# Kernel optimization log

Hardware: AMD Instinct MI355X
Metric: run time of the kernel (lower is better)

## Reference

```python
import jax, jax.numpy as jnp
import numpy as np

STRIDE = 8
PAD = 8
KSZ = 16


def setup_inputs() -> dict:
    key = jax.random.key(0)
    k1, k2, k3 = jax.random.split(key, 3)
    B, Cin, Cout, L = 16, 512, 1, 4000
    inp = jax.random.normal(k1, (B, Cin, L), dtype=jnp.float32)
    # t60 in [0.1, 0.5) so that round(t60*100)-10 lands in [0, 40]
    t60s = 0.1 + 0.39 * jax.random.uniform(k2, (B // 2,), dtype=jnp.float32)
    kernel_weight = jax.random.uniform(k3, (41, Cin, Cout, KSZ), dtype=jnp.float32)
    return {"input": inp, "t60s": t60s, "kernel_weight": kernel_weight}


def reference(input, t60s, kernel_weight):
    # per-sample kernel index: round(t60*100).int().repeat(2) - 10
    idx = jnp.tile(jnp.round(t60s * 100.0).astype(jnp.int32), 2) - 10  # (B,)
    w = kernel_weight[idx]                      # (B, Cin, Cout, K) gathered per sample
    # torch conv_transpose1d(x, W) == conv(x with lhs_dilation=stride,
    #                                      flip_k(W).swap(Cin,Cout), pad=K-1-p)
    w = jnp.flip(jnp.swapaxes(w, 1, 2), axis=-1)  # (B, Cout, Cin, K)
    pad = KSZ - 1 - PAD

    def per_sample(x, wk):  # x: (Cin, L), wk: (Cout, Cin, K)
        y = jax.lax.conv_general_dilated(
            x[None], wk,
            window_strides=(1,),
            padding=[(pad, pad)],
            lhs_dilation=(STRIDE,),
            dimension_numbers=("NCH", "OIH", "NCH"),
        )
        return y[0]  # (Cout, L_out), L_out = (L-1)*stride - 2*PAD + K

    return jax.vmap(per_sample)(input, w)  # (B, Cout, L_out)
```

## Files before the change

### kernel.cpp

```cpp
#include <hip/hip_runtime.h>

#define L_IN   4000
#define CIN    512
#define KSZ    16
#define LOUT   31992
#define NQ     3999
#define QPB    256
#define RST    1152

__global__ __launch_bounds__(1024, 4)
void dereverb_kernel(const float* __restrict__ x,
                     const float* __restrict__ t60s,
                     const float* __restrict__ kw,
                     float* __restrict__ out)
{
    __shared__ float lds[8 * RST];

    const int b    = blockIdx.y;
    const int q0   = blockIdx.x * QPB;
    const int tid  = threadIdx.x;
    const int lane = tid & 63;
    const int wave = tid >> 6;

    float t60 = t60s[b & 7];
    int kidx = (int)rintf(t60 * 100.0f) - 10;
    kidx = __builtin_amdgcn_readfirstlane(kidx);
    const float4* wsrc = (const float4*)(kw + (size_t)kidx * (CIN * KSZ));

    ((float4*)lds)[tid]        = wsrc[tid];
    ((float4*)lds)[tid + 1024] = wsrc[tid + 1024];
    __syncthreads();

    const float* xb = x + ((size_t)b * CIN + wave * 32) * L_IN;
    const float* xp[4];
    #pragma unroll
    for (int qi = 0; qi < 4; ++qi) {
        int q  = q0 + qi * 64 + lane;
        int qc = q < NQ - 1 ? q : (NQ - 1);
        xp[qi] = xb + qc;
    }

    const float4* wl = (const float4*)(lds + wave * 32 * KSZ);

    float acc[4][8];
    #pragma unroll
    for (int qi = 0; qi < 4; ++qi)
        #pragma unroll
        for (int r = 0; r < 8; ++r) acc[qi][r] = 0.0f;

    #pragma unroll 4
    for (int ci = 0; ci < 32; ++ci) {
        float x0[4], x1[4];
        #pragma unroll
        for (int qi = 0; qi < 4; ++qi) {
            x0[qi] = xp[qi][0];
            x1[qi] = xp[qi][1];
            xp[qi] += L_IN;
        }
        float4 wv[4];
        wv[0] = wl[0];
        wv[1] = wl[1];
        wv[2] = wl[2];
        wv[3] = wl[3];
        wl += 4;
        const float* wf = (const float*)wv;
        #pragma unroll
        for (int qi = 0; qi < 4; ++qi)
            #pragma unroll
            for (int r = 0; r < 8; ++r) {
                acc[qi][r] = fmaf(x1[qi], wf[r],     acc[qi][r]);
                acc[qi][r] = fmaf(x0[qi], wf[r + 8], acc[qi][r]);
            }
    }

    #pragma unroll
    for (int qi = 0; qi < 4; ++qi)
        if (q0 + qi * 64 + lane > NQ - 1)
            #pragma unroll
            for (int r = 0; r < 8; ++r) acc[qi][r] = 0.0f;

    const size_t obase = (size_t)b * LOUT + (size_t)q0 * 8;
    #pragma unroll
    for (int p = 0; p < 2; ++p) {
        __syncthreads();
        if (wave >= 8) {
            #pragma unroll
            for (int h = 0; h < 2; ++h) {
                float* rp = lds + (wave - 8) * RST + 9 * (h * 64 + lane);
                #pragma unroll
                for (int r = 0; r < 8; ++r) rp[r] = acc[2 * p + h][r];
            }
        }
        __syncthreads();
        if (wave < 8) {
            #pragma unroll
            for (int h = 0; h < 2; ++h) {
                float* rp = lds + wave * RST + 9 * (h * 64 + lane);
                #pragma unroll
                for (int r = 0; r < 8; ++r) rp[r] += acc[2 * p + h][r];
            }
        }
        __syncthreads();
        int tl = p * 1024 + tid;
        if (q0 * 8 + tl < LOUT) {
            int ql = tid >> 3, r = tid & 7;
            float s = 0.0f;
            #pragma unroll
            for (int w = 0; w < 8; ++w)
                s += lds[w * RST + 9 * ql + r];
            out[obase + tl] = s;
        }
    }
}

extern "C" void kernel_launch(void* const* d_in, const int* in_sizes, int n_in,
                              void* d_out, int out_size, void* d_ws, size_t ws_size,
                              hipStream_t stream) {
    const float* x    = (const float*)d_in[0];
    const float* t60s = (const float*)d_in[1];
    const float* kw   = (const float*)d_in[2];
    float* out = (float*)d_out;

    dim3 grid((NQ + QPB - 1) / QPB, 16);
    dereverb_kernel<<<grid, 1024, 0, stream>>>(x, t60s, kw, out);
}
```

Baseline: 195.6 us.

## Assign four contiguous output positions per lane and load inputs as float4

Each lane now owns four adjacent input positions instead of four positions spaced 64 apart. Per channel it loads them with one float4 plus one scalar for the neighbour sample, replacing eight scalar loads. The LDS reduction layout is reworked to match (stride 17 per lane, new row stride), and the final store mapping changes so each thread writes a 16-element chunk. This cuts the number of global load instructions, at the cost of a less coalesced float4 access across lanes and an extra boundary load.

```diff
diff --git a/kernel.cpp b/kernel.cpp
--- a/kernel.cpp
+++ b/kernel.cpp
@@ -6,7 +6,7 @@
 #define LOUT   31992
 #define NQ     3999
 #define QPB    256
-#define RST    1152
+#define RST    1088
 
 __global__ __launch_bounds__(1024, 4)
 void dereverb_kernel(const float* __restrict__ x,
@@ -31,14 +31,13 @@
     ((float4*)lds)[tid + 1024] = wsrc[tid + 1024];
     __syncthreads();
 
-    const float* xb = x + ((size_t)b * CIN + wave * 32) * L_IN;
-    const float* xp[4];
-    #pragma unroll
-    for (int qi = 0; qi < 4; ++qi) {
-        int q  = q0 + qi * 64 + lane;
-        int qc = q < NQ - 1 ? q : (NQ - 1);
-        xp[qi] = xb + qc;
-    }
+    const int qb  = q0 + 4 * lane;
+    const int qbl = qb < 3996 ? qb : 3996;
+    const int qan = (qb + 4) < NQ ? (qb + 4) : NQ;
+
+    const float* xr = x + ((size_t)b * CIN + wave * 32) * L_IN;
+    const float* xp = xr + qbl;
+    const float* xq = xr + qan;
 
     const float4* wl = (const float4*)(lds + wave * 32 * KSZ);
 
@@ -50,13 +49,11 @@
 
     #pragma unroll 4
     for (int ci = 0; ci < 32; ++ci) {
-        float x0[4], x1[4];
-        #pragma unroll
-        for (int qi = 0; qi < 4; ++qi) {
-            x0[qi] = xp[qi][0];
-            x1[qi] = xp[qi][1];
-            xp[qi] += L_IN;
-        }
+        float4 a  = *(const float4*)xp;
+        float  an = *xq;
+        xp += L_IN;
+        xq += L_IN;
+
         float4 wv[4];
         wv[0] = wl[0];
         wv[1] = wl[1];
@@ -64,18 +61,21 @@
         wv[3] = wl[3];
         wl += 4;
         const float* wf = (const float*)wv;
+
+        const float x0v[4] = {a.x, a.y, a.z, a.w};
+        const float x1v[4] = {a.y, a.z, a.w, an};
         #pragma unroll
         for (int qi = 0; qi < 4; ++qi)
             #pragma unroll
             for (int r = 0; r < 8; ++r) {
-                acc[qi][r] = fmaf(x1[qi], wf[r],     acc[qi][r]);
-                acc[qi][r] = fmaf(x0[qi], wf[r + 8], acc[qi][r]);
+                acc[qi][r] = fmaf(x1v[qi], wf[r],     acc[qi][r]);
+                acc[qi][r] = fmaf(x0v[qi], wf[r + 8], acc[qi][r]);
             }
     }
 
     #pragma unroll
     for (int qi = 0; qi < 4; ++qi)
-        if (q0 + qi * 64 + lane > NQ - 1)
+        if (qb + qi > NQ - 1)
             #pragma unroll
             for (int r = 0; r < 8; ++r) acc[qi][r] = 0.0f;
 
@@ -84,30 +84,30 @@
     for (int p = 0; p < 2; ++p) {
         __syncthreads();
         if (wave >= 8) {
+            float* rp = lds + (wave - 8) * RST + lane * 17;
             #pragma unroll
-            for (int h = 0; h < 2; ++h) {
-                float* rp = lds + (wave - 8) * RST + 9 * (h * 64 + lane);
+            for (int qih = 0; qih < 2; ++qih)
                 #pragma unroll
-                for (int r = 0; r < 8; ++r) rp[r] = acc[2 * p + h][r];
-            }
+                for (int r = 0; r < 8; ++r)
+                    rp[qih * 8 + r] = acc[2 * p + qih][r];
         }
         __syncthreads();
         if (wave < 8) {
+            float* rp = lds + wave * RST + lane * 17;
             #pragma unroll
-            for (int h = 0; h < 2; ++h) {
-                float* rp = lds + wave * RST + 9 * (h * 64 + lane);
+            for (int qih = 0; qih < 2; ++qih)
                 #pragma unroll
-                for (int r = 0; r < 8; ++r) rp[r] += acc[2 * p + h][r];
-            }
+                for (int r = 0; r < 8; ++r)
+                    rp[qih * 8 + r] += acc[2 * p + qih][r];
         }
         __syncthreads();
-        int tl = p * 1024 + tid;
+        int k = tid >> 4, j = tid & 15;
+        int tl = 32 * k + 16 * p + j;
         if (q0 * 8 + tl < LOUT) {
-            int ql = tid >> 3, r = tid & 7;
             float s = 0.0f;
             #pragma unroll
             for (int w = 0; w < 8; ++w)
-                s += lds[w * RST + 9 * ql + r];
+                s += lds[w * RST + k * 17 + j];
             out[obase + tl] = s;
         }
     }
```

After: 190.4 us. 2.6% less time.
